# Optimization experiments

Measured on AMD Instinct MI355X. Metric: run time of the kernel, lower is better.

The kernel has to match this reference:

```python
import jax, jax.numpy as jnp
import numpy as np

B, H, W_IMG, C = 256, 88, 88, 3
NUM_CH = 64
MATCH_ATOL = 0.0


def setup_inputs() -> dict:
    key = jax.random.key(0)
    k1, k2 = jax.random.split(key)
    rgb = jax.random.randint(k1, (B, H, W_IMG, C), 0, 256, dtype=jnp.int32)
    # conv params: HWIO layout for lax.conv_general_dilated
    Wc = jax.random.normal(k2, (8, 8, C, NUM_CH), dtype=jnp.float32) * 0.05
    bc = jnp.zeros((NUM_CH,), dtype=jnp.float32)
    return {"rgb": rgb, "Wc": Wc, "bc": bc}


def _guidance_from_feats(out):
    # out: [B, 121, 64]
    # pairwise feature-equality counts (O(N^2) broadcast, as in original)
    eq = jnp.max(jnp.abs(out[:, None, :, :] - out[:, :, None, :]), axis=-1) <= MATCH_ATOL
    counts = jnp.sum(eq, axis=-1)  # [B, 121] int32, always >= 1 (self-match)
    M = counts.shape[-1]
    hist = jax.vmap(lambda c: jnp.bincount(c, length=M + 1))(counts)  # [B, M+1]
    cum = jnp.cumsum(hist, axis=-1)
    K = int(0.3 * M)
    allow_freq = cum <= K
    kmin = jnp.min(counts, axis=-1)  # [B]
    allow_freq = jnp.logical_or(allow_freq, jnp.arange(M + 1)[None, :] == kmin[:, None])
    # gather allow flag per position via its count value
    mask_keep = jnp.take_along_axis(allow_freq[:, None, :], counts[..., None], axis=-1)[..., 0]
    fcounts = counts.astype(jnp.float32)
    logits = jnp.where(mask_keep, -jnp.log(fcounts), -jnp.inf)
    attn = jax.nn.softmax(logits, axis=-1)  # [B, 121]
    guidance = attn.reshape(attn.shape[0], 1, 11, 11)
    return jax.lax.stop_gradient(guidance)


def reference(rgb, Wc, bc):
    x = rgb.astype(jnp.float32) / 255.0  # [B, 88, 88, 3]
    feats = jax.lax.conv_general_dilated(
        x, Wc, window_strides=(8, 8), padding='VALID',
        dimension_numbers=('NHWC', 'HWIO', 'NHWC')) + bc
    feats = jax.nn.relu(feats)  # [B, 11, 11, 64]
    vis_op = feats.reshape(feats.shape[0], -1, feats.shape[-1])  # [B, 121, 64]
    guidance = _guidance_from_feats(vis_op)  # [B, 1, 11, 11]
    return (vis_op, guidance)
```

## Files before the change

### kernel.cpp

```cpp
#include <hip/hip_runtime.h>
#include <hip/hip_bf16.h>

#define B_SZ 256
#define NCH 64
#define NPOS 121
#define NPATCH (B_SZ * NPOS)
#define KTOT 192
#define RGB_W 264
#define LDR 264
#define LDB 200
#define FST 68

typedef short bf16x8 __attribute__((ext_vector_type(8)));
typedef float f32x4 __attribute__((ext_vector_type(4)));

static __device__ inline unsigned f2bf(float x) {
  union { float f; unsigned u; } a; a.f = x;
  return (a.u + 0x7FFFu + ((a.u >> 16) & 1u)) >> 16;
}
static __device__ inline unsigned pack2(float lo, float hi) {
  return f2bf(lo) | (f2bf(hi) << 16);
}

__global__ __launch_bounds__(512) void fused(
    const int* __restrict__ rgb, const float* __restrict__ Wc,
    const float* __restrict__ bc, float* __restrict__ out,
    float* __restrict__ gout) {
  __shared__ __align__(16) unsigned short rgbL[88 * LDR];
  __shared__ __align__(16) unsigned short BtL[NCH * LDB];
  __shared__ unsigned sig[NPOS];
  __shared__ int counts[NPOS];
  __shared__ int redi[8];
  __shared__ float redf[8];
  unsigned* fbits = (unsigned*)rgbL;

  const int b = blockIdx.x, tid = threadIdx.x;
  const int lane = tid & 63, w = tid >> 6;
  const int lr = lane & 15, lg = lane >> 4;

  {
    #pragma unroll
    for (int j = 0; j < 12; ++j) {
      const int k = w * 24 + 2 * j;
      const float w0 = Wc[k * NCH + lane];
      const float w1 = Wc[(k + 1) * NCH + lane];
      *(unsigned*)&BtL[lane * LDB + k] = pack2(w0, w1);
    }
  }

  const int4* src4 = (const int4*)(rgb + (size_t)b * 88 * RGB_W);
  int4 r[11];
  #pragma unroll
  for (int it = 0; it < 11; ++it) r[it] = src4[tid + it * 512];
  int4 rt;
  const bool tail = (tid < 176);
  if (tail) rt = src4[5632 + tid];
  #pragma unroll
  for (int it = 0; it < 11; ++it) {
    const int i = tid + it * 512;
    const int e = i * 4, row = e / RGB_W, col = e - row * RGB_W;
    uint2 p;
    p.x = pack2((float)r[it].x * (1.f/255.f), (float)r[it].y * (1.f/255.f));
    p.y = pack2((float)r[it].z * (1.f/255.f), (float)r[it].w * (1.f/255.f));
    *(uint2*)&rgbL[row * LDR + col] = p;
  }
  if (tail) {
    const int i = 5632 + tid;
    const int e = i * 4, row = e / RGB_W, col = e - row * RGB_W;
    uint2 p;
    p.x = pack2((float)rt.x * (1.f/255.f), (float)rt.y * (1.f/255.f));
    p.y = pack2((float)rt.z * (1.f/255.f), (float)rt.w * (1.f/255.f));
    *(uint2*)&rgbL[row * LDR + col] = p;
  }
  __syncthreads();

  const int p = w * 16 + lr;
  const int pe = p > 120 ? 120 : p;
  const int oy = pe / 11, ox = pe - oy * 11;
  f32x4 acc[4] = {};
  #pragma unroll
  for (int ks = 0; ks < 6; ++ks) {
    const int k0 = ks * 32 + lg * 8;
    const int ky = k0 / 24, km = k0 - ky * 24;
    const bf16x8 a = *(const bf16x8*)&rgbL[(oy * 8 + ky) * LDR + ox * 24 + km];
    #pragma unroll
    for (int ni = 0; ni < 4; ++ni) {
      const bf16x8 bb = *(const bf16x8*)&BtL[(ni * 16 + lr) * LDB + k0];
      acc[ni] = __builtin_amdgcn_mfma_f32_16x16x32_bf16(a, bb, acc[ni], 0, 0, 0);
    }
  }
  __syncthreads();

  float bias[4];
  #pragma unroll
  for (int ni = 0; ni < 4; ++ni) bias[ni] = bc[ni * 16 + lr];
  float* outB = out + (size_t)b * NPOS * NCH;
  #pragma unroll
  for (int rr = 0; rr < 4; ++rr) {
    const int ps = w * 16 + lg * 4 + rr;
    if (ps < NPOS) {
      #pragma unroll
      for (int ni = 0; ni < 4; ++ni) {
        const float v = fmaxf(acc[ni][rr] + bias[ni], 0.f) + 0.f;
        outB[ps * NCH + ni * 16 + lr] = v;
        fbits[ps * FST + ni * 16 + lr] = __float_as_uint(v);
      }
    }
  }
  __syncthreads();

  if (tid < NPOS) {
    const uint4* fr = (const uint4*)&fbits[tid * FST];
    unsigned h = 0;
    #pragma unroll
    for (int q = 0; q < 16; ++q) {
      const uint4 v = fr[q];
      h ^= (v.x ^ (v.x >> 15)) * ((8u*q + 1u) * 0x9E3779B9u);
      h ^= (v.y ^ (v.y >> 15)) * ((8u*q + 3u) * 0x9E3779B9u);
      h ^= (v.z ^ (v.z >> 15)) * ((8u*q + 5u) * 0x9E3779B9u);
      h ^= (v.w ^ (v.w >> 15)) * ((8u*q + 7u) * 0x9E3779B9u);
    }
    sig[tid] = h;
  }
  __syncthreads();

  int cnt = 0x7fffffff;
  if (tid < NPOS) {
    const unsigned si = sig[tid];
    int m = 0;
    for (int j = 0; j < NPOS; ++j) m += (sig[j] == si) ? 1 : 0;
    cnt = 1;
    if (m > 1) {
      cnt = 0;
      for (int j = 0; j < NPOS; ++j) {
        if (sig[j] == si) {
          int eq = 1;
          for (int c = 0; c < NCH; ++c) eq &= (fbits[tid*FST + c] == fbits[j*FST + c]);
          cnt += eq;
        }
      }
    }
    counts[tid] = cnt;
  }
  __syncthreads();

  int km_ = cnt;
  #pragma unroll
  for (int off = 1; off < 64; off <<= 1) km_ = min(km_, __shfl_xor(km_, off, 64));
  if (lane == 0) redi[w] = km_;
  __syncthreads();
  int kmin = redi[0];
  #pragma unroll
  for (int q = 1; q < 8; ++q) kmin = min(kmin, redi[q]);

  float wv = 0.f;
  if (tid < NPOS) {
    int cum = 0;
    for (int j = 0; j < NPOS; ++j) cum += (counts[j] <= cnt) ? 1 : 0;
    if (cum <= 36 || cnt == kmin) wv = 1.f / (float)cnt;
  }
  float s = wv;
  #pragma unroll
  for (int off = 1; off < 64; off <<= 1) s += __shfl_xor(s, off, 64);
  if (lane == 0) redf[w] = s;
  __syncthreads();
  float Z = redf[0];
  #pragma unroll
  for (int q = 1; q < 8; ++q) Z += redf[q];
  if (tid < NPOS) gout[(size_t)b * NPOS + tid] = wv / Z;
}

extern "C" void kernel_launch(void* const* d_in, const int* in_sizes, int n_in,
                              void* d_out, int out_size, void* d_ws, size_t ws_size,
                              hipStream_t stream) {
  const int*   rgb = (const int*)d_in[0];
  const float* Wc  = (const float*)d_in[1];
  const float* bc  = (const float*)d_in[2];
  float* out   = (float*)d_out;
  float* guide = out + (size_t)NPATCH * NCH;

  fused<<<B_SZ, 512, 0, stream>>>(rgb, Wc, bc, out, guide);
}
```

Before: 77.79 us.

## Compute row hashes in MFMA epilogue via shuffles and use lighter barriers

The per-position signature hash is now computed in the conv epilogue: each lane hashes its four channels and a 16-lane xor shuffle reduces them, replacing a separate serial pass over shared memory. Two __syncthreads are dropped, and the rest become LDS-only waits plus s_barrier, so the barrier does not wait on outstanding global stores. Weight staging is moved after the rgb loads are issued and bias loads are hoisted, letting global latency overlap. The hash function itself changes (different multipliers per channel), which is acceptable only because equal features still hash equally and equality is verified exactly.

```diff
diff --git a/kernel.cpp b/kernel.cpp
--- a/kernel.cpp
+++ b/kernel.cpp
@@ -22,6 +22,12 @@
   return f2bf(lo) | (f2bf(hi) << 16);
 }
 
+static __device__ inline void light_barrier() {
+  asm volatile("s_waitcnt lgkmcnt(0)" ::: "memory");
+  __builtin_amdgcn_s_barrier();
+  asm volatile("" ::: "memory");
+}
+
 __global__ __launch_bounds__(512) void fused(
     const int* __restrict__ rgb, const float* __restrict__ Wc,
     const float* __restrict__ bc, float* __restrict__ out,
@@ -38,15 +44,9 @@
   const int lane = tid & 63, w = tid >> 6;
   const int lr = lane & 15, lg = lane >> 4;
 
-  {
-    #pragma unroll
-    for (int j = 0; j < 12; ++j) {
-      const int k = w * 24 + 2 * j;
-      const float w0 = Wc[k * NCH + lane];
-      const float w1 = Wc[(k + 1) * NCH + lane];
-      *(unsigned*)&BtL[lane * LDB + k] = pack2(w0, w1);
-    }
-  }
+  float bias[4];
+  #pragma unroll
+  for (int ni = 0; ni < 4; ++ni) bias[ni] = bc[ni * 16 + lr];
 
   const int4* src4 = (const int4*)(rgb + (size_t)b * 88 * RGB_W);
   int4 r[11];
@@ -55,6 +55,14 @@
   int4 rt;
   const bool tail = (tid < 176);
   if (tail) rt = src4[5632 + tid];
+
+  #pragma unroll
+  for (int j = 0; j < 12; ++j) {
+    const int k = w * 24 + 2 * j;
+    *(unsigned*)&BtL[lane * LDB + k] =
+        pack2(Wc[k * NCH + lane], Wc[(k + 1) * NCH + lane]);
+  }
+
   #pragma unroll
   for (int it = 0; it < 11; ++it) {
     const int i = tid + it * 512;
@@ -91,38 +99,30 @@
   }
   __syncthreads();
 
-  float bias[4];
+  unsigned mult[4];
   #pragma unroll
-  for (int ni = 0; ni < 4; ++ni) bias[ni] = bc[ni * 16 + lr];
+  for (int ni = 0; ni < 4; ++ni)
+    mult[ni] = (2u * (unsigned)(ni * 16 + lr) + 1u) * 0x9E3779B9u;
   float* outB = out + (size_t)b * NPOS * NCH;
   #pragma unroll
   for (int rr = 0; rr < 4; ++rr) {
     const int ps = w * 16 + lg * 4 + rr;
     if (ps < NPOS) {
+      unsigned ph = 0;
       #pragma unroll
       for (int ni = 0; ni < 4; ++ni) {
         const float v = fmaxf(acc[ni][rr] + bias[ni], 0.f) + 0.f;
+        const unsigned bits = __float_as_uint(v);
         outB[ps * NCH + ni * 16 + lr] = v;
-        fbits[ps * FST + ni * 16 + lr] = __float_as_uint(v);
+        fbits[ps * FST + ni * 16 + lr] = bits;
+        ph ^= (bits ^ (bits >> 15)) * mult[ni];
       }
+      #pragma unroll
+      for (int m = 1; m < 16; m <<= 1) ph ^= __shfl_xor(ph, m, 64);
+      if (lr == 0) sig[ps] = ph;
     }
   }
-  __syncthreads();
-
-  if (tid < NPOS) {
-    const uint4* fr = (const uint4*)&fbits[tid * FST];
-    unsigned h = 0;
-    #pragma unroll
-    for (int q = 0; q < 16; ++q) {
-      const uint4 v = fr[q];
-      h ^= (v.x ^ (v.x >> 15)) * ((8u*q + 1u) * 0x9E3779B9u);
-      h ^= (v.y ^ (v.y >> 15)) * ((8u*q + 3u) * 0x9E3779B9u);
-      h ^= (v.z ^ (v.z >> 15)) * ((8u*q + 5u) * 0x9E3779B9u);
-      h ^= (v.w ^ (v.w >> 15)) * ((8u*q + 7u) * 0x9E3779B9u);
-    }
-    sig[tid] = h;
-  }
-  __syncthreads();
+  light_barrier();
 
   int cnt = 0x7fffffff;
   if (tid < NPOS) {
@@ -142,13 +142,11 @@
     }
     counts[tid] = cnt;
   }
-  __syncthreads();
-
   int km_ = cnt;
   #pragma unroll
-  for (int off = 1; off < 64; off <<= 1) km_ = min(km_, __shfl_xor(km_, off, 64));
+  for (int m = 1; m < 64; m <<= 1) km_ = min(km_, __shfl_xor(km_, m, 64));
   if (lane == 0) redi[w] = km_;
-  __syncthreads();
+  light_barrier();
   int kmin = redi[0];
   #pragma unroll
   for (int q = 1; q < 8; ++q) kmin = min(kmin, redi[q]);
@@ -161,9 +159,9 @@
   }
   float s = wv;
   #pragma unroll
-  for (int off = 1; off < 64; off <<= 1) s += __shfl_xor(s, off, 64);
+  for (int m = 1; m < 64; m <<= 1) s += __shfl_xor(s, m, 64);
   if (lane == 0) redf[w] = s;
-  __syncthreads();
+  light_barrier();
   float Z = redf[0];
   #pragma unroll
   for (int q = 1; q < 8; ++q) Z += redf[q];
```

New measurement: 78.62 us. Within noise of the previous version (+1.1%).

## Split fused kernel into half-image conv blocks and a separate guidance kernel

Applied to the files above, without the earlier changes.

The single fused kernel (one 512-thread block per image) is replaced by two kernels. A conv kernel runs two 256-thread blocks per image, each staging only the 48 rows it needs, and a guidance kernel reloads the features from global memory to do the hashing, counting and softmax. This doubles the number of conv blocks and frees the conv block from the serial guidance phase. In exchange it adds a second launch and a global-memory round trip of the features.

```diff
diff --git a/kernel.cpp b/kernel.cpp
--- a/kernel.cpp
+++ b/kernel.cpp
@@ -10,6 +10,7 @@
 #define LDR 264
 #define LDB 200
 #define FST 68
+#define CROWS 48
 
 typedef short bf16x8 __attribute__((ext_vector_type(8)));
 typedef float f32x4 __attribute__((ext_vector_type(4)));
@@ -22,59 +23,58 @@
   return f2bf(lo) | (f2bf(hi) << 16);
 }
 
-__global__ __launch_bounds__(512) void fused(
+__global__ __launch_bounds__(256) void conv_mfma(
     const int* __restrict__ rgb, const float* __restrict__ Wc,
-    const float* __restrict__ bc, float* __restrict__ out,
-    float* __restrict__ gout) {
-  __shared__ __align__(16) unsigned short rgbL[88 * LDR];
+    const float* __restrict__ bc, float* __restrict__ out) {
+  __shared__ __align__(16) unsigned short imgL[CROWS * LDR];
   __shared__ __align__(16) unsigned short BtL[NCH * LDB];
-  __shared__ unsigned sig[NPOS];
-  __shared__ int counts[NPOS];
-  __shared__ int redi[8];
-  __shared__ float redf[8];
-  unsigned* fbits = (unsigned*)rgbL;
-
-  const int b = blockIdx.x, tid = threadIdx.x;
-  const int lane = tid & 63, w = tid >> 6;
+
+  const int blk = blockIdx.x;
+  const int b = blk >> 1, half = blk & 1;
+  const int tid = threadIdx.x, lane = tid & 63, w = tid >> 6;
   const int lr = lane & 15, lg = lane >> 4;
-
-  {
-    #pragma unroll
-    for (int j = 0; j < 12; ++j) {
-      const int k = w * 24 + 2 * j;
-      const float w0 = Wc[k * NCH + lane];
-      const float w1 = Wc[(k + 1) * NCH + lane];
-      *(unsigned*)&BtL[lane * LDB + k] = pack2(w0, w1);
-    }
-  }
-
-  const int4* src4 = (const int4*)(rgb + (size_t)b * 88 * RGB_W);
-  int4 r[11];
-  #pragma unroll
-  for (int it = 0; it < 11; ++it) r[it] = src4[tid + it * 512];
+  const int rowbase = half ? 40 : 0;
+  const int pbase = half ? 64 : 0;
+
+  float bias[4];
+  #pragma unroll
+  for (int ni = 0; ni < 4; ++ni) bias[ni] = bc[ni * 16 + lr];
+
+  const int4* src4 = (const int4*)(rgb + ((size_t)b * 88 + rowbase) * RGB_W);
+  int4 r[12];
+  #pragma unroll
+  for (int it = 0; it < 12; ++it) r[it] = src4[tid + it * 256];
   int4 rt;
-  const bool tail = (tid < 176);
-  if (tail) rt = src4[5632 + tid];
-  #pragma unroll
-  for (int it = 0; it < 11; ++it) {
-    const int i = tid + it * 512;
+  const bool tail = (tid < 96);
+  if (tail) rt = src4[3072 + tid];
+
+  #pragma unroll
+  for (int j = 0; j < 24; ++j) {
+    const int k = w * 48 + 2 * j;
+    *(unsigned*)&BtL[lane * LDB + k] =
+        pack2(Wc[k * NCH + lane], Wc[(k + 1) * NCH + lane]);
+  }
+
+  #pragma unroll
+  for (int it = 0; it < 12; ++it) {
+    const int i = tid + it * 256;
     const int e = i * 4, row = e / RGB_W, col = e - row * RGB_W;
     uint2 p;
     p.x = pack2((float)r[it].x * (1.f/255.f), (float)r[it].y * (1.f/255.f));
     p.y = pack2((float)r[it].z * (1.f/255.f), (float)r[it].w * (1.f/255.f));
-    *(uint2*)&rgbL[row * LDR + col] = p;
+    *(uint2*)&imgL[row * LDR + col] = p;
   }
   if (tail) {
-    const int i = 5632 + tid;
+    const int i = 3072 + tid;
     const int e = i * 4, row = e / RGB_W, col = e - row * RGB_W;
     uint2 p;
     p.x = pack2((float)rt.x * (1.f/255.f), (float)rt.y * (1.f/255.f));
     p.y = pack2((float)rt.z * (1.f/255.f), (float)rt.w * (1.f/255.f));
-    *(uint2*)&rgbL[row * LDR + col] = p;
-  }
-  __syncthreads();
-
-  const int p = w * 16 + lr;
+    *(uint2*)&imgL[row * LDR + col] = p;
+  }
+  __syncthreads();
+
+  const int p = pbase + w * 16 + lr;
   const int pe = p > 120 ? 120 : p;
   const int oy = pe / 11, ox = pe - oy * 11;
   f32x4 acc[4] = {};
@@ -82,30 +82,55 @@
   for (int ks = 0; ks < 6; ++ks) {
     const int k0 = ks * 32 + lg * 8;
     const int ky = k0 / 24, km = k0 - ky * 24;
-    const bf16x8 a = *(const bf16x8*)&rgbL[(oy * 8 + ky) * LDR + ox * 24 + km];
+    const bf16x8 a =
+        *(const bf16x8*)&imgL[(oy * 8 + ky - rowbase) * LDR + ox * 24 + km];
     #pragma unroll
     for (int ni = 0; ni < 4; ++ni) {
       const bf16x8 bb = *(const bf16x8*)&BtL[(ni * 16 + lr) * LDB + k0];
       acc[ni] = __builtin_amdgcn_mfma_f32_16x16x32_bf16(a, bb, acc[ni], 0, 0, 0);
     }
   }
-  __syncthreads();
-
-  float bias[4];
-  #pragma unroll
-  for (int ni = 0; ni < 4; ++ni) bias[ni] = bc[ni * 16 + lr];
+
   float* outB = out + (size_t)b * NPOS * NCH;
   #pragma unroll
   for (int rr = 0; rr < 4; ++rr) {
-    const int ps = w * 16 + lg * 4 + rr;
+    const int ps = pbase + w * 16 + lg * 4 + rr;
     if (ps < NPOS) {
       #pragma unroll
       for (int ni = 0; ni < 4; ++ni) {
         const float v = fmaxf(acc[ni][rr] + bias[ni], 0.f) + 0.f;
         outB[ps * NCH + ni * 16 + lr] = v;
-        fbits[ps * FST + ni * 16 + lr] = __float_as_uint(v);
       }
     }
+  }
+}
+
+__global__ __launch_bounds__(256) void guide(
+    const float* __restrict__ feats, float* __restrict__ gout) {
+  __shared__ __align__(16) unsigned fbits[NPOS * FST];
+  __shared__ unsigned sig[NPOS];
+  __shared__ int counts[NPOS];
+  __shared__ int redi[4];
+  __shared__ float redf[4];
+
+  const int b = blockIdx.x, tid = threadIdx.x;
+  const int lane = tid & 63, w = tid >> 6;
+
+  const uint4* src = (const uint4*)(feats + (size_t)b * NPOS * NCH);
+  uint4 v[7];
+  #pragma unroll
+  for (int it = 0; it < 7; ++it) v[it] = src[tid + it * 256];
+  uint4 vt;
+  const bool tail = (tid < 144);
+  if (tail) vt = src[1792 + tid];
+  #pragma unroll
+  for (int it = 0; it < 7; ++it) {
+    const int g = tid + it * 256, row = g >> 4, q = g & 15;
+    *(uint4*)&fbits[row * FST + q * 4] = v[it];
+  }
+  if (tail) {
+    const int g = 1792 + tid, row = g >> 4, q = g & 15;
+    *(uint4*)&fbits[row * FST + q * 4] = vt;
   }
   __syncthreads();
 
@@ -114,11 +139,11 @@
     unsigned h = 0;
     #pragma unroll
     for (int q = 0; q < 16; ++q) {
-      const uint4 v = fr[q];
-      h ^= (v.x ^ (v.x >> 15)) * ((8u*q + 1u) * 0x9E3779B9u);
-      h ^= (v.y ^ (v.y >> 15)) * ((8u*q + 3u) * 0x9E3779B9u);
-      h ^= (v.z ^ (v.z >> 15)) * ((8u*q + 5u) * 0x9E3779B9u);
-      h ^= (v.w ^ (v.w >> 15)) * ((8u*q + 7u) * 0x9E3779B9u);
+      const uint4 u = fr[q];
+      h ^= (u.x ^ (u.x >> 15)) * ((8u*q + 1u) * 0x9E3779B9u);
+      h ^= (u.y ^ (u.y >> 15)) * ((8u*q + 3u) * 0x9E3779B9u);
+      h ^= (u.z ^ (u.z >> 15)) * ((8u*q + 5u) * 0x9E3779B9u);
+      h ^= (u.w ^ (u.w >> 15)) * ((8u*q + 7u) * 0x9E3779B9u);
     }
     sig[tid] = h;
   }
@@ -142,16 +167,12 @@
     }
     counts[tid] = cnt;
   }
-  __syncthreads();
-
   int km_ = cnt;
   #pragma unroll
-  for (int off = 1; off < 64; off <<= 1) km_ = min(km_, __shfl_xor(km_, off, 64));
+  for (int m = 1; m < 64; m <<= 1) km_ = min(km_, __shfl_xor(km_, m, 64));
   if (lane == 0) redi[w] = km_;
   __syncthreads();
-  int kmin = redi[0];
-  #pragma unroll
-  for (int q = 1; q < 8; ++q) kmin = min(kmin, redi[q]);
+  int kmin = min(min(redi[0], redi[1]), min(redi[2], redi[3]));
 
   float wv = 0.f;
   if (tid < NPOS) {
@@ -161,12 +182,10 @@
   }
   float s = wv;
   #pragma unroll
-  for (int off = 1; off < 64; off <<= 1) s += __shfl_xor(s, off, 64);
+  for (int m = 1; m < 64; m <<= 1) s += __shfl_xor(s, m, 64);
   if (lane == 0) redf[w] = s;
   __syncthreads();
-  float Z = redf[0];
-  #pragma unroll
-  for (int q = 1; q < 8; ++q) Z += redf[q];
+  const float Z = redf[0] + redf[1] + redf[2] + redf[3];
   if (tid < NPOS) gout[(size_t)b * NPOS + tid] = wv / Z;
 }
 
@@ -177,7 +196,8 @@
   const float* Wc  = (const float*)d_in[1];
   const float* bc  = (const float*)d_in[2];
   float* out   = (float*)d_out;
-  float* guide = out + (size_t)NPATCH * NCH;
-
-  fused<<<B_SZ, 512, 0, stream>>>(rgb, Wc, bc, out, guide);
-}
+  float* guide_o = out + (size_t)NPATCH * NCH;
+
+  conv_mfma<<<2 * B_SZ, 256, 0, stream>>>(rgb, Wc, bc, out);
+  guide<<<B_SZ, 256, 0, stream>>>(out, guide_o);
+}
```

Result: slower. 80.23 us (+3.1%).
